# Kernel optimization log

Hardware: AMD Instinct MI355X
Metric: run time of the kernel (lower is better)

Reference implementation:

```python
import jax, jax.numpy as jnp
import numpy as np

N, E, F, C, ED, G, D = 50000, 1000000, 30, 64, 11, 1024, 256


def setup_inputs() -> dict:
    key = jax.random.key(0)
    ks = jax.random.split(key, 20)
    rn = lambda k, shape, s=0.1: jax.random.normal(k, shape, jnp.float32) * s
    return {
        "x": rn(ks[0], (N, F), 1.0),
        "edge_attr": jax.random.uniform(ks[1], (E, ED), jnp.float32),
        "W0": rn(ks[2], (F, C)), "asrc0": rn(ks[3], (C,)), "adst0": rn(ks[4], (C,)),
        "We0": rn(ks[5], (ED, C)), "ae0": rn(ks[6], (C,)), "Wres0": rn(ks[7], (F, C)),
        "b0": jnp.zeros((C,), jnp.float32),
        "W": rn(ks[8], (3, C, C)), "asrc": rn(ks[9], (3, C)), "adst": rn(ks[10], (3, C)),
        "We": rn(ks[11], (3, ED, C)), "ae": rn(ks[12], (3, C)), "Wres": rn(ks[13], (3, C, C)),
        "b": jnp.zeros((3, C), jnp.float32),
        "Wout": rn(ks[14], (2 * C, D)), "bout": jnp.zeros((D,), jnp.float32),
        "edge_index": jax.random.randint(ks[15], (2, E), 0, N),
        "batch_index": jnp.sort(jax.random.randint(ks[16], (N,), 0, G)),
    }


def _gat(x, src, dst, edge_attr, W, asrc, adst, We, ae, Wres, b):
    """PyG GATConv (heads=1) with edge_dim and residual=True."""
    n = x.shape[0]
    h = x @ W                                   # [N, C]
    e = edge_attr @ We                          # [E, C]
    alpha = (jnp.sum(h * asrc, -1)[src]
             + jnp.sum(h * adst, -1)[dst]
             + jnp.sum(e * ae, -1))             # [E]
    alpha = jax.nn.leaky_relu(alpha, 0.2)
    m = jax.ops.segment_max(alpha, dst, num_segments=n)
    a = jnp.exp(alpha - m[dst])
    s = jax.ops.segment_sum(a, dst, num_segments=n)
    a = a / (s[dst] + 1e-16)                    # per-dst softmax
    out = jax.ops.segment_sum(a[:, None] * h[src], dst, num_segments=n)
    return out + x @ Wres + b


def reference(x, edge_attr, W0, asrc0, adst0, We0, ae0, Wres0, b0,
              W, asrc, adst, We, ae, Wres, b, Wout, bout,
              edge_index, batch_index):
    src, dst = edge_index[0], edge_index[1]
    h = jax.nn.leaky_relu(
        _gat(x, src, dst, edge_attr, W0, asrc0, adst0, We0, ae0, Wres0, b0), 0.01)
    for i in range(3):  # conv1..conv3 (fixed small layer loop)
        h = _gat(h, src, dst, edge_attr, W[i], asrc[i], adst[i],
                 We[i], ae[i], Wres[i], b[i])
        if i < 2:
            h = jax.nn.leaky_relu(h, 0.01)
    gmax = jax.ops.segment_max(h, batch_index, num_segments=G)
    gmax = jnp.where(jnp.isfinite(gmax), gmax, 0.0)  # empty graphs -> 0
    cnt = jax.ops.segment_sum(jnp.ones((h.shape[0],), h.dtype), batch_index,
                              num_segments=G)
    gmean = jax.ops.segment_sum(h, batch_index, num_segments=G) / jnp.maximum(cnt, 1.0)[:, None]
    pooled = jax.nn.leaky_relu(jnp.concatenate([gmax, gmean], axis=1), 0.01)
    return pooled @ Wout + bout
```

## Files before the change

### kernel.cpp

```cpp
#include <hip/hip_runtime.h>
#include <hip/hip_fp16.h>

#define NN 50000
#define NE 1000000
#define FIN0 30
#define C 64
#define ED 11
#define NG 1024
#define DOUT 256
#define NBIN 196
#define PA_EDGES 1024

typedef unsigned long long ull;

__global__ __launch_bounds__(256) void hist196_kernel(const int* __restrict__ dst,
    int* __restrict__ bcnt){
  __shared__ int h[256];
  int t=threadIdx.x;
  h[t]=0;
  __syncthreads();
  for(int i=blockIdx.x*256+t;i<NE;i+=gridDim.x*256)
    atomicAdd(&h[dst[i]>>8],1);
  __syncthreads();
  if(h[t]) atomicAdd(&bcnt[t],h[t]);
}

__global__ __launch_bounds__(256) void scan196_kernel(const int* __restrict__ bcnt,
    int* __restrict__ bbase, int* __restrict__ gcur){
  __shared__ int p[256];
  int t=threadIdx.x;
  int v=bcnt[t];
  p[t]=v; __syncthreads();
  #pragma unroll
  for(int off=1;off<256;off<<=1){
    int u=(t>=off)?p[t-off]:0;
    __syncthreads(); p[t]+=u; __syncthreads();
  }
  int ex=p[t]-v;
  if(t<=NBIN) bbase[t]=ex;
  if(t<NBIN)  gcur[t]=ex;
}

__global__ __launch_bounds__(256) void grow_kernel(const int* __restrict__ batch,
    int* __restrict__ growptr){
  int i=blockIdx.x*256+threadIdx.x;
  if(i>=NN) return;
  int bi=batch[i];
  int bp=(i==0)?-1:batch[i-1];
  for(int g=bp+1;g<=bi;++g) growptr[g]=i;
  if(i==NN-1){ for(int g=bi+1;g<=NG;++g) growptr[g]=NN; }
}

__global__ __launch_bounds__(256) void part_kernel(const int* __restrict__ dst,
    const int* __restrict__ src, const float* __restrict__ edge_attr,
    const float* __restrict__ We0, const float* __restrict__ ae0,
    const float* __restrict__ We,  const float* __restrict__ ae,
    int* __restrict__ gcur, uint4* __restrict__ prec){
  __shared__ uint4 lrec[PA_EDGES];
  __shared__ float sw[4][ED];
  __shared__ int hist[256], sc[256], lofs[256], bb[256];
  __shared__ int wsum[4];
  int t=threadIdx.x;
  hist[t]=0;
  if(t<4*ED){
    int l=t/ED, j=t%ED;
    const float* wp=(l==0)? (We0+(size_t)j*C) : (We+((size_t)(l-1)*ED+j)*C);
    const float* ap=(l==0)? ae0 : (ae+(size_t)(l-1)*C);
    float s=0.f;
    for(int c=0;c<C;++c) s+=wp[c]*ap[c];
    sw[l][j]=s;
  }
  __syncthreads();
  size_t e0=(size_t)blockIdx.x*PA_EDGES;
  int cnt=(int)min((size_t)PA_EDGES,(size_t)NE-e0);
  int dreg[4], sreg[4];
  #pragma unroll
  for(int r=0;r<4;++r){
    int i=r*256+t;
    if(i<cnt){
      dreg[r]=dst[e0+i]; sreg[r]=src[e0+i];
      atomicAdd(&hist[dreg[r]>>8],1);
    } else dreg[r]=-1;
  }
  __syncthreads();
  int v=hist[t];
  int inc=v;
  #pragma unroll
  for(int off=1;off<64;off<<=1){
    int u=__shfl_up(inc,off,64);
    if((t&63)>=off) inc+=u;
  }
  if((t&63)==63) wsum[t>>6]=inc;
  __syncthreads();
  int woff=0;
  int myw=t>>6;
  #pragma unroll
  for(int k=0;k<3;++k) if(k<myw) woff+=wsum[k];
  int ex=woff+inc-v;
  sc[t]=ex;
  lofs[t]=ex;
  bb[t]=(v>0)?atomicAdd(&gcur[t],v):0;
  __syncthreads();
  #pragma unroll
  for(int r=0;r<4;++r){
    int i=r*256+t;
    if(i<cnt){
      const float* ea=edge_attr+(e0+i)*(size_t)ED;
      float d0=0,d1=0,d2=0,d3=0;
      #pragma unroll
      for(int j=0;j<ED;++j){
        float ev=ea[j];
        d0=fmaf(ev,sw[0][j],d0);
        d1=fmaf(ev,sw[1][j],d1);
        d2=fmaf(ev,sw[2][j],d2);
        d3=fmaf(ev,sw[3][j],d3);
      }
      uint4 rec;
      rec.x=(unsigned)dreg[r]; rec.y=(unsigned)sreg[r];
      rec.z=(unsigned)__half_as_ushort(__float2half(d0))
           |((unsigned)__half_as_ushort(__float2half(d1))<<16);
      rec.w=(unsigned)__half_as_ushort(__float2half(d2))
           |((unsigned)__half_as_ushort(__float2half(d3))<<16);
      int slot=atomicAdd(&lofs[dreg[r]>>8],1);
      lrec[slot]=rec;
    }
  }
  __syncthreads();
  for(int i=t;i<cnt;i+=256){
    uint4 rec=lrec[i];
    int b=(int)(rec.x>>8);
    int g=bb[b]+i-sc[b];
    prec[g]=rec;
  }
}

__global__ __launch_bounds__(256) void build_kernel(const uint4* __restrict__ prec,
    const int* __restrict__ bbase,
    int* __restrict__ rowptr, int* __restrict__ src_csr, ushort* __restrict__ edch){
  __shared__ int cnt[256], p[256], cur[256];
  int t=threadIdx.x, b=blockIdx.x;
  int n0=b<<8;
  cnt[t]=0;
  __syncthreads();
  int beg=bbase[b], endd=bbase[b+1];
  for(int j=beg+t;j<endd;j+=256)
    atomicAdd(&cnt[(int)prec[j].x-n0],1);
  __syncthreads();
  int v=cnt[t];
  p[t]=v; __syncthreads();
  #pragma unroll
  for(int off=1;off<256;off<<=1){
    int u=(t>=off)?p[t-off]:0;
    __syncthreads(); p[t]+=u; __syncthreads();
  }
  int ex=p[t]-v;
  cur[t]=beg+ex;
  if(n0+t<NN) rowptr[n0+t]=beg+ex;
  if(b==0&&t==0) rowptr[NN]=NE;
  __syncthreads();
  for(int j=beg+t;j<endd;j+=256){
    uint4 r=prec[j];
    int d=(int)r.x, s=(int)r.y;
    int pos=atomicAdd(&cur[d-n0],1);
    src_csr[pos]=s;
    edch[pos]                =(ushort)(r.z&0xffffu);
    edch[(size_t)NE+pos]     =(ushort)(r.z>>16);
    edch[2*(size_t)NE+pos]   =(ushort)(r.w&0xffffu);
    edch[3*(size_t)NE+pos]   =(ushort)(r.w>>16);
  }
}

template<int FIN, int SXS>
__global__ __launch_bounds__(256) void feat_kernel(const float* __restrict__ in,
    const float* __restrict__ W, const float* __restrict__ Wres,
    const float* __restrict__ bvec, const float* __restrict__ av_src,
    const float* __restrict__ av_dst,
    __half* __restrict__ hW16, float* __restrict__ outb,
    float* __restrict__ as_, float* __restrict__ ad_){
  __shared__ float sW[FIN*C], sR[FIN*C];
  __shared__ float sx[64*SXS];
  __shared__ float sb[C], ss[C], sd[C];
  int tid=threadIdx.x;
  if(tid<C){ sb[tid]=bvec[tid]; ss[tid]=av_src[tid]; sd[tid]=av_dst[tid]; }
  for(int i=tid;i<FIN*C;i+=256){ sW[i]=W[i]; sR[i]=Wres[i]; }
  int nbase=blockIdx.x*64;
  int nvalid=min(64,NN-nbase);
  if constexpr (FIN==64){
    const float4* in4=(const float4*)(in+(size_t)nbase*64);
    for(int i=tid;i<1024;i+=256){
      int n=i>>4, k=(i&15)*4;
      float4 v=(n<nvalid)?in4[i]:make_float4(0.f,0.f,0.f,0.f);
      *(float4*)&sx[n*SXS+k]=v;
    }
  } else {
    for(int i=tid;i<64*FIN;i+=256){
      int n=i/FIN, k=i-n*FIN;
      sx[n*SXS+k]=(n<nvalid)?in[(size_t)(nbase+n)*FIN+k]:0.f;
    }
  }
  __syncthreads();
  int w=tid>>6, lane=tid&63;
  int ng=lane>>4, cl=lane&15;
  int n0=w*16+ng*4;
  int c0=cl*4;
  float hw[4][4]={}, hr[4][4]={};
  const float* sxp=&sx[n0*SXS];
  #pragma unroll 2
  for(int k=0;k<FIN;k+=2){
    float4 wv0=*(const float4*)&sW[k*C+c0];
    float4 rv0=*(const float4*)&sR[k*C+c0];
    float4 wv1=*(const float4*)&sW[(k+1)*C+c0];
    float4 rv1=*(const float4*)&sR[(k+1)*C+c0];
    float2 x0=*(const float2*)&sxp[k];
    float2 x1=*(const float2*)&sxp[SXS+k];
    float2 x2=*(const float2*)&sxp[2*SXS+k];
    float2 x3=*(const float2*)&sxp[3*SXS+k];
    float xa[4]={x0.x,x1.x,x2.x,x3.x};
    float xb[4]={x0.y,x1.y,x2.y,x3.y};
    #pragma unroll
    for(int r=0;r<4;++r){
      hw[r][0]=fmaf(xa[r],wv0.x,hw[r][0]);
      hw[r][1]=fmaf(xa[r],wv0.y,hw[r][1]);
      hw[r][2]=fmaf(xa[r],wv0.z,hw[r][2]);
      hw[r][3]=fmaf(xa[r],wv0.w,hw[r][3]);
      hr[r][0]=fmaf(xa[r],rv0.x,hr[r][0]);
      hr[r][1]=fmaf(xa[r],rv0.y,hr[r][1]);
      hr[r][2]=fmaf(xa[r],rv0.z,hr[r][2]);
      hr[r][3]=fmaf(xa[r],rv0.w,hr[r][3]);
      hw[r][0]=fmaf(xb[r],wv1.x,hw[r][0]);
      hw[r][1]=fmaf(xb[r],wv1.y,hw[r][1]);
      hw[r][2]=fmaf(xb[r],wv1.z,hw[r][2]);
      hw[r][3]=fmaf(xb[r],wv1.w,hw[r][3]);
      hr[r][0]=fmaf(xb[r],rv1.x,hr[r][0]);
      hr[r][1]=fmaf(xb[r],rv1.y,hr[r][1]);
      hr[r][2]=fmaf(xb[r],rv1.z,hr[r][2]);
      hr[r][3]=fmaf(xb[r],rv1.w,hr[r][3]);
    }
  }
  float s0=ss[c0], s1=ss[c0+1], s2=ss[c0+2], s3=ss[c0+3];
  float d0=sd[c0], d1=sd[c0+1], d2=sd[c0+2], d3=sd[c0+3];
  float b0v=sb[c0], b1v=sb[c0+1], b2v=sb[c0+2], b3v=sb[c0+3];
  #pragma unroll
  for(int r=0;r<4;++r){
    int n=n0+r;
    float ps=hw[r][0]*s0+hw[r][1]*s1+hw[r][2]*s2+hw[r][3]*s3;
    float pd=hw[r][0]*d0+hw[r][1]*d1+hw[r][2]*d2+hw[r][3]*d3;
    #pragma unroll
    for(int off=1;off<16;off<<=1){ ps+=__shfl_xor(ps,off,64); pd+=__shfl_xor(pd,off,64); }
    if(n<nvalid){
      size_t gn=(size_t)(nbase+n);
      ushort4 hv;
      hv.x=__half_as_ushort(__float2half(hw[r][0]));
      hv.y=__half_as_ushort(__float2half(hw[r][1]));
      hv.z=__half_as_ushort(__float2half(hw[r][2]));
      hv.w=__half_as_ushort(__float2half(hw[r][3]));
      *(ushort4*)&hW16[gn*C+c0]=hv;
      float4 ov;
      ov.x=hr[r][0]+b0v; ov.y=hr[r][1]+b1v; ov.z=hr[r][2]+b2v; ov.w=hr[r][3]+b3v;
      *(float4*)&outb[gn*C+c0]=ov;
      if(cl==0){ as_[gn]=ps; ad_[gn]=pd; }
    }
  }
}

__device__ __forceinline__ void acc8(float* a, float at, uint4 u){
  __half2 h0=*(__half2*)&u.x, h1=*(__half2*)&u.y, h2=*(__half2*)&u.z, h3=*(__half2*)&u.w;
  float2 f0=__half22float2(h0), f1=__half22float2(h1);
  float2 f2=__half22float2(h2), f3=__half22float2(h3);
  a[0]=fmaf(at,f0.x,a[0]); a[1]=fmaf(at,f0.y,a[1]);
  a[2]=fmaf(at,f1.x,a[2]); a[3]=fmaf(at,f1.y,a[3]);
  a[4]=fmaf(at,f2.x,a[4]); a[5]=fmaf(at,f2.y,a[5]);
  a[6]=fmaf(at,f3.x,a[6]); a[7]=fmaf(at,f3.y,a[7]);
}

__global__ __launch_bounds__(256) void agg_kernel(const int* __restrict__ rowptr,
    const int* __restrict__ src_csr, const ushort* __restrict__ edc_l,
    const float* __restrict__ as_, const float* __restrict__ ad_,
    const __half* __restrict__ hW16, float* __restrict__ outb, int relu){
  __shared__ float2 sws[4][64];
  int w=threadIdx.x>>6, lane=threadIdx.x&63;
  int half=lane>>5, hl=lane&31;
  int n0=blockIdx.x*8+w*2;
  int nidx=n0+half;
  int beg=rowptr[nidx], end=rowptr[nidx+1];
  int deg=end-beg;
  const uint4* hw4=(const uint4*)hW16;

  if(__all(deg<=32)){
    float ad_n=ad_[nidx];
    int j=beg+hl;
    float al=-INFINITY; int sl=0;
    if(hl<deg){
      sl=src_csr[j];
      float a=as_[sl]+ad_n+__half2float(__ushort_as_half(edc_l[j]));
      al=(a>0.f)?a:0.2f*a;
    }
    float mn=al;
    #pragma unroll
    for(int off=16;off;off>>=1) mn=fmaxf(mn,__shfl_xor(mn,off,64));
    float wl=(hl<deg)?__expf(al-mn):0.f;
    float s=wl;
    #pragma unroll
    for(int off=16;off;off>>=1) s+=__shfl_xor(s,off,64);
    float2 pr; pr.x=wl; pr.y=__int_as_float(sl);
    sws[w][lane]=pr;
    int g=hl>>3, gl=hl&7;
    float acc[8]={0.f,0.f,0.f,0.f,0.f,0.f,0.f,0.f};
    int base=half*32;
    int t=g;
    for(; t+4<deg; t+=8){
      float2 r0=sws[w][base+t], r1=sws[w][base+t+4];
      uint4 u0=hw4[(size_t)__float_as_int(r0.y)*8+gl];
      uint4 u1=hw4[(size_t)__float_as_int(r1.y)*8+gl];
      acc8(acc,r0.x,u0);
      acc8(acc,r1.x,u1);
    }
    if(t<deg){
      float2 r=sws[w][base+t];
      uint4 u=hw4[(size_t)__float_as_int(r.y)*8+gl];
      acc8(acc,r.x,u);
    }
    #pragma unroll
    for(int off=8;off<=16;off<<=1){
      #pragma unroll
      for(int i=0;i<8;++i) acc[i]+=__shfl_xor(acc[i],off,64);
    }
    if(hl<8){
      float denom=s+1e-16f;
      size_t o0=(size_t)nidx*C+hl*8;
      float4 oa=*(float4*)&outb[o0];
      float4 ob=*(float4*)&outb[o0+4];
      float4 va,vb;
      va.x=acc[0]/denom+oa.x; va.y=acc[1]/denom+oa.y;
      va.z=acc[2]/denom+oa.z; va.w=acc[3]/denom+oa.w;
      vb.x=acc[4]/denom+ob.x; vb.y=acc[5]/denom+ob.y;
      vb.z=acc[6]/denom+ob.z; vb.w=acc[7]/denom+ob.w;
      if(relu){
        va.x=(va.x>0.f)?va.x:0.01f*va.x; va.y=(va.y>0.f)?va.y:0.01f*va.y;
        va.z=(va.z>0.f)?va.z:0.01f*va.z; va.w=(va.w>0.f)?va.w:0.01f*va.w;
        vb.x=(vb.x>0.f)?vb.x:0.01f*vb.x; vb.y=(vb.y>0.f)?vb.y:0.01f*vb.y;
        vb.z=(vb.z>0.f)?vb.z:0.01f*vb.z; vb.w=(vb.w>0.f)?vb.w:0.01f*vb.w;
      }
      *(float4*)&outb[o0]=va;
      *(float4*)&outb[o0+4]=vb;
    }
    return;
  }

  for(int h=0;h<2;++h){
    int m=n0+h;
    int bh=__shfl(beg,h*32,64);
    int dh=__shfl(deg,h*32,64);
    float ad_n=ad_[m];
    int g2=lane>>3, gl2=lane&7;
    float s=0.f;
    float acc[8]={0.f,0.f,0.f,0.f,0.f,0.f,0.f,0.f};
    if(dh<=64){
      int j=bh+lane;
      float al=-INFINITY; int sl=0;
      if(lane<dh){
        sl=src_csr[j];
        float a=as_[sl]+ad_n+__half2float(__ushort_as_half(edc_l[j]));
        al=(a>0.f)?a:0.2f*a;
      }
      float mn=al;
      #pragma unroll
      for(int off=32;off;off>>=1) mn=fmaxf(mn,__shfl_xor(mn,off,64));
      float wl=(lane<dh)?__expf(al-mn):0.f;
      s=wl;
      #pragma unroll
      for(int off=32;off;off>>=1) s+=__shfl_xor(s,off,64);
      float2 pr; pr.x=wl; pr.y=__int_as_float(sl);
      sws[w][lane]=pr;
      int t=g2;
      for(; t+8<dh; t+=16){
        float2 r0=sws[w][t], r1=sws[w][t+8];
        uint4 u0=hw4[(size_t)__float_as_int(r0.y)*8+gl2];
        uint4 u1=hw4[(size_t)__float_as_int(r1.y)*8+gl2];
        acc8(acc,r0.x,u0);
        acc8(acc,r1.x,u1);
      }
      if(t<dh){
        float2 r=sws[w][t];
        uint4 u=hw4[(size_t)__float_as_int(r.y)*8+gl2];
        acc8(acc,r.x,u);
      }
    } else {
      float m_=-INFINITY;
      for(int base=bh;base<bh+dh;base+=64){
        int j=base+lane;
        float al=-INFINITY; int sl=0;
        if(j<bh+dh){
          sl=src_csr[j];
          float a=as_[sl]+ad_n+__half2float(__ushort_as_half(edc_l[j]));
          al=(a>0.f)?a:0.2f*a;
        }
        float cm=al;
        #pragma unroll
        for(int off=32;off;off>>=1) cm=fmaxf(cm,__shfl_xor(cm,off,64));
        float mn=fmaxf(m_,cm);
        float scale=(m_==-INFINITY)?0.f:__expf(m_-mn);
        s*=scale;
        #pragma unroll
        for(int i=0;i<8;++i) acc[i]*=scale;
        float wl=(j<bh+dh)?__expf(al-mn):0.f;
        float cs=wl;
        #pragma unroll
        for(int off=32;off;off>>=1) cs+=__shfl_xor(cs,off,64);
        s+=cs; m_=mn;
        float2 pr; pr.x=wl; pr.y=__int_as_float(sl);
        sws[w][lane]=pr;
        int cnt=min(64,bh+dh-base);
        int t=g2;
        for(; t+8<cnt; t+=16){
          float2 r0=sws[w][t], r1=sws[w][t+8];
          uint4 u0=hw4[(size_t)__float_as_int(r0.y)*8+gl2];
          uint4 u1=hw4[(size_t)__float_as_int(r1.y)*8+gl2];
          acc8(acc,r0.x,u0);
          acc8(acc,r1.x,u1);
        }
        if(t<cnt){
          float2 r=sws[w][t];
          uint4 u=hw4[(size_t)__float_as_int(r.y)*8+gl2];
          acc8(acc,r.x,u);
        }
      }
    }
    #pragma unroll
    for(int off=8;off<64;off<<=1){
      #pragma unroll
      for(int i=0;i<8;++i) acc[i]+=__shfl_xor(acc[i],off,64);
    }
    if(g2==0){
      float denom=s+1e-16f;
      size_t o0=(size_t)m*C+gl2*8;
      float4 oa=*(float4*)&outb[o0];
      float4 ob=*(float4*)&outb[o0+4];
      float4 va,vb;
      va.x=acc[0]/denom+oa.x; va.y=acc[1]/denom+oa.y;
      va.z=acc[2]/denom+oa.z; va.w=acc[3]/denom+oa.w;
      vb.x=acc[4]/denom+ob.x; vb.y=acc[5]/denom+ob.y;
      vb.z=acc[6]/denom+ob.z; vb.w=acc[7]/denom+ob.w;
      if(relu){
        va.x=(va.x>0.f)?va.x:0.01f*va.x; va.y=(va.y>0.f)?va.y:0.01f*va.y;
        va.z=(va.z>0.f)?va.z:0.01f*va.z; va.w=(va.w>0.f)?va.w:0.01f*va.w;
        vb.x=(vb.x>0.f)?vb.x:0.01f*vb.x; vb.y=(vb.y>0.f)?vb.y:0.01f*vb.y;
        vb.z=(vb.z>0.f)?vb.z:0.01f*vb.z; vb.w=(vb.w>0.f)?vb.w:0.01f*vb.w;
      }
      *(float4*)&outb[o0]=va;
      *(float4*)&outb[o0+4]=vb;
    }
  }
}

__global__ __launch_bounds__(256) void pool_kernel(const float* __restrict__ h,
    const int* __restrict__ growptr, float* __restrict__ pooled){
  int w=threadIdx.x>>6, lane=threadIdx.x&63;
  int g=blockIdx.x*4+w;
  if(g>=NG) return;
  int beg=growptr[g], end=growptr[g+1];
  float mx=-INFINITY, sm=0.f;
  for(int n=beg;n<end;++n){ float v=h[(size_t)n*C+lane]; mx=fmaxf(mx,v); sm+=v; }
  int cnt=end-beg;
  float gm=(cnt==0)?0.f:mx;
  float mean=sm/fmaxf((float)cnt,1.f);
  gm=(gm>0.f)?gm:0.01f*gm;
  mean=(mean>0.f)?mean:0.01f*mean;
  pooled[(size_t)g*128+lane]=gm;
  pooled[(size_t)g*128+64+lane]=mean;
}

__global__ __launch_bounds__(256) void out_kernel(const float* __restrict__ pooled,
    const float* __restrict__ Wout, const float* __restrict__ bout,
    float* __restrict__ out){
  __shared__ float sp[128];
  int g=blockIdx.x, d=threadIdx.x;
  if(d<128) sp[d]=pooled[(size_t)g*128+d];
  __syncthreads();
  float o=bout[d];
  for(int k=0;k<128;++k) o=fmaf(sp[k],Wout[k*DOUT+d],o);
  out[(size_t)g*DOUT+d]=o;
}

extern "C" void kernel_launch(void* const* d_in, const int* in_sizes, int n_in,
                              void* d_out, int out_size, void* d_ws, size_t ws_size,
                              hipStream_t stream){
  const float* x        =(const float*)d_in[0];
  const float* edge_attr=(const float*)d_in[1];
  const float* W0       =(const float*)d_in[2];
  const float* asrc0    =(const float*)d_in[3];
  const float* adst0    =(const float*)d_in[4];
  const float* We0      =(const float*)d_in[5];
  const float* ae0      =(const float*)d_in[6];
  const float* Wres0    =(const float*)d_in[7];
  const float* b0       =(const float*)d_in[8];
  const float* W        =(const float*)d_in[9];
  const float* asrc     =(const float*)d_in[10];
  const float* adst     =(const float*)d_in[11];
  const float* We       =(const float*)d_in[12];
  const float* ae       =(const float*)d_in[13];
  const float* Wres     =(const float*)d_in[14];
  const float* b        =(const float*)d_in[15];
  const float* Wout     =(const float*)d_in[16];
  const float* bout     =(const float*)d_in[17];
  const int* edge_index =(const int*)d_in[18];
  const int* batch_index=(const int*)d_in[19];
  const int* src=edge_index;
  const int* dst=edge_index+NE;

  char* p=(char*)d_ws;
  auto take=[&](size_t bytes)->void*{ void* r=(void*)p; p+=(bytes+255)&~(size_t)255; return r; };
  int* rowptr  =(int*)take((size_t)(NN+1)*4);
  int* growptr =(int*)take((size_t)(NG+1)*4);
  int* bcnt    =(int*)take((size_t)256*4);
  int* bbase   =(int*)take((size_t)256*4);
  int* gcur    =(int*)take((size_t)256*4);
  int* src_csr =(int*)take((size_t)NE*4);
  float* as_   =(float*)take((size_t)NN*4);
  float* ad_   =(float*)take((size_t)NN*4);
  ushort* edch =(ushort*)take((size_t)NE*4*2);
  __half* hW16 =(__half*)take((size_t)NN*C*2);
  float* bufA  =(float*)take((size_t)NN*C*4);
  uint4* prec  =(uint4*)take((size_t)NE*16);
  float* bufB  =(float*)prec;
  float* pooled=(float*)take((size_t)NG*128*4);
  (void)ws_size; (void)in_sizes; (void)n_in; (void)out_size;

  hipMemsetAsync(bcnt,0,(size_t)256*4,stream);
  hist196_kernel<<<1024,256,0,stream>>>(dst,bcnt);
  scan196_kernel<<<1,256,0,stream>>>(bcnt,bbase,gcur);
  grow_kernel<<<(NN+255)/256,256,0,stream>>>(batch_index,growptr);

  part_kernel<<<(NE+PA_EDGES-1)/PA_EDGES,256,0,stream>>>(dst,src,edge_attr,
      We0,ae0,We,ae,gcur,prec);
  build_kernel<<<NBIN,256,0,stream>>>(prec,bbase,rowptr,src_csr,edch);

  const int nblkF=(NN+63)/64;
  const int nblkA=NN/8;
  feat_kernel<FIN0,36><<<nblkF,256,0,stream>>>(x,W0,Wres0,b0,asrc0,adst0,hW16,bufA,as_,ad_);
  agg_kernel<<<nblkA,256,0,stream>>>(rowptr,src_csr,edch,as_,ad_,hW16,bufA,1);
  float* bin=bufA; float* bo=bufB;
  for(int i=0;i<3;++i){
    feat_kernel<C,68><<<nblkF,256,0,stream>>>(bin,W+(size_t)i*C*C,Wres+(size_t)i*C*C,
        b+(size_t)i*C,asrc+(size_t)i*C,adst+(size_t)i*C,hW16,bo,as_,ad_);
    agg_kernel<<<nblkA,256,0,stream>>>(rowptr,src_csr,edch+(size_t)(i+1)*NE,as_,ad_,hW16,bo,(i<2)?1:0);
    float* t=bin; bin=bo; bo=t;
  }
  pool_kernel<<<(NG+3)/4,256,0,stream>>>(bin,growptr,pooled);
  out_kernel<<<NG,256,0,stream>>>(pooled,Wout,bout,(float*)d_out);
}
```

Before: 307.7 us.

## Split aggregation into softmax-weight kernel and channel-split gather kernel

Replaces the fused per-node softmax+gather aggregation with two kernels. One computes normalized edge weights into a global buffer, and the other gathers source features with the channel dimension split across two block halves, so each lane reads 32 of the 64 channels. The aim is more parallelism and simpler, more uniform gather loops. The cost is an extra kernel launch per layer, an extra write and read of a 4-byte weight per edge, and rowptr/src_csr being read twice. The partition kernel's edges per block are also halved.

```diff
diff --git a/kernel.cpp b/kernel.cpp
--- a/kernel.cpp
+++ b/kernel.cpp
@@ -9,7 +9,8 @@
 #define NG 1024
 #define DOUT 256
 #define NBIN 196
-#define PA_EDGES 1024
+#define PA_EDGES 512
+#define GHB (NN/8)
 
 typedef unsigned long long ull;
 
@@ -73,9 +74,9 @@
   __syncthreads();
   size_t e0=(size_t)blockIdx.x*PA_EDGES;
   int cnt=(int)min((size_t)PA_EDGES,(size_t)NE-e0);
-  int dreg[4], sreg[4];
-  #pragma unroll
-  for(int r=0;r<4;++r){
+  int dreg[2], sreg[2];
+  #pragma unroll
+  for(int r=0;r<2;++r){
     int i=r*256+t;
     if(i<cnt){
       dreg[r]=dst[e0+i]; sreg[r]=src[e0+i];
@@ -102,7 +103,7 @@
   bb[t]=(v>0)?atomicAdd(&gcur[t],v):0;
   __syncthreads();
   #pragma unroll
-  for(int r=0;r<4;++r){
+  for(int r=0;r<2;++r){
     int i=r*256+t;
     if(i<cnt){
       const float* ea=edge_attr+(e0+i)*(size_t)ED;
@@ -263,6 +264,79 @@
   }
 }
 
+__global__ __launch_bounds__(256) void wcalc_kernel(const int* __restrict__ rowptr,
+    const int* __restrict__ src_csr, const ushort* __restrict__ edc_l,
+    const float* __restrict__ as_, const float* __restrict__ ad_,
+    float* __restrict__ wgt){
+  int w=threadIdx.x>>6, lane=threadIdx.x&63;
+  int half=lane>>5, hl=lane&31;
+  int n0=blockIdx.x*8+w*2;
+  int nidx=n0+half;
+  int beg=rowptr[nidx], end=rowptr[nidx+1];
+  int deg=end-beg;
+
+  if(__all(deg<=32)){
+    int j=beg+hl;
+    float al=-INFINITY;
+    if(hl<deg){
+      int sl=src_csr[j];
+      float a=as_[sl]+ad_[nidx]+__half2float(__ushort_as_half(edc_l[j]));
+      al=(a>0.f)?a:0.2f*a;
+    }
+    float mn=al;
+    #pragma unroll
+    for(int off=16;off;off>>=1) mn=fmaxf(mn,__shfl_xor(mn,off,64));
+    float wl=(hl<deg)?__expf(al-mn):0.f;
+    float s=wl;
+    #pragma unroll
+    for(int off=16;off;off>>=1) s+=__shfl_xor(s,off,64);
+    if(hl<deg) wgt[j]=wl/(s+1e-16f);
+    return;
+  }
+
+  for(int h=0;h<2;++h){
+    int m=n0+h;
+    int bh=__shfl(beg,h*32,64);
+    int dh=__shfl(deg,h*32,64);
+    int eh=bh+dh;
+    float ad_n=ad_[m];
+    float mx=-INFINITY;
+    for(int base=bh;base<eh;base+=64){
+      int j=base+lane;
+      float al=-INFINITY;
+      if(j<eh){
+        int sl=src_csr[j];
+        float a=as_[sl]+ad_n+__half2float(__ushort_as_half(edc_l[j]));
+        al=(a>0.f)?a:0.2f*a;
+      }
+      #pragma unroll
+      for(int off=32;off;off>>=1) al=fmaxf(al,__shfl_xor(al,off,64));
+      mx=fmaxf(mx,al);
+    }
+    float s=0.f;
+    for(int base=bh;base<eh;base+=64){
+      int j=base+lane;
+      float wl=0.f;
+      if(j<eh){
+        int sl=src_csr[j];
+        float a=as_[sl]+ad_n+__half2float(__ushort_as_half(edc_l[j]));
+        float al=(a>0.f)?a:0.2f*a;
+        wl=__expf(al-mx);
+        wgt[j]=wl;
+      }
+      float cs=wl;
+      #pragma unroll
+      for(int off=32;off;off>>=1) cs+=__shfl_xor(cs,off,64);
+      s+=cs;
+    }
+    float inv=1.f/(s+1e-16f);
+    for(int base=bh;base<eh;base+=64){
+      int j=base+lane;
+      if(j<eh) wgt[j]*=inv;
+    }
+  }
+}
+
 __device__ __forceinline__ void acc8(float* a, float at, uint4 u){
   __half2 h0=*(__half2*)&u.x, h1=*(__half2*)&u.y, h2=*(__half2*)&u.z, h3=*(__half2*)&u.w;
   float2 f0=__half22float2(h0), f1=__half22float2(h1);
@@ -273,183 +347,57 @@
   a[6]=fmaf(at,f3.x,a[6]); a[7]=fmaf(at,f3.y,a[7]);
 }
 
-__global__ __launch_bounds__(256) void agg_kernel(const int* __restrict__ rowptr,
-    const int* __restrict__ src_csr, const ushort* __restrict__ edc_l,
-    const float* __restrict__ as_, const float* __restrict__ ad_,
+__global__ __launch_bounds__(256) void gath_kernel(const int* __restrict__ rowptr,
+    const int* __restrict__ src_csr, const float* __restrict__ wgt,
     const __half* __restrict__ hW16, float* __restrict__ outb, int relu){
-  __shared__ float2 sws[4][64];
   int w=threadIdx.x>>6, lane=threadIdx.x&63;
   int half=lane>>5, hl=lane&31;
-  int n0=blockIdx.x*8+w*2;
-  int nidx=n0+half;
-  int beg=rowptr[nidx], end=rowptr[nidx+1];
-  int deg=end-beg;
+  int cb=blockIdx.x;
+  int chalf=0;
+  if(cb>=GHB){ chalf=1; cb-=GHB; }
+  int nidx=cb*8+w*2+half;
+  int beg=rowptr[nidx];
+  int deg=rowptr[nidx+1]-beg;
+  int g=hl>>2, gl=hl&3;
   const uint4* hw4=(const uint4*)hW16;
-
-  if(__all(deg<=32)){
-    float ad_n=ad_[nidx];
-    int j=beg+hl;
-    float al=-INFINITY; int sl=0;
-    if(hl<deg){
-      sl=src_csr[j];
-      float a=as_[sl]+ad_n+__half2float(__ushort_as_half(edc_l[j]));
-      al=(a>0.f)?a:0.2f*a;
-    }
-    float mn=al;
+  size_t rowoff=(size_t)(chalf*4+gl);
+  float acc[8]={0.f,0.f,0.f,0.f,0.f,0.f,0.f,0.f};
+  int t=g;
+  for(; t+8<deg; t+=16){
+    int j0=beg+t, j1=beg+t+8;
+    float w0=wgt[j0], w1=wgt[j1];
+    int s0=src_csr[j0], s1=src_csr[j1];
+    uint4 u0=hw4[(size_t)s0*8+rowoff];
+    uint4 u1=hw4[(size_t)s1*8+rowoff];
+    acc8(acc,w0,u0);
+    acc8(acc,w1,u1);
+  }
+  if(t<deg){
+    int j=beg+t;
+    float wv=wgt[j]; int sv=src_csr[j];
+    uint4 u=hw4[(size_t)sv*8+rowoff];
+    acc8(acc,wv,u);
+  }
+  #pragma unroll
+  for(int off=4;off<=16;off<<=1){
     #pragma unroll
-    for(int off=16;off;off>>=1) mn=fmaxf(mn,__shfl_xor(mn,off,64));
-    float wl=(hl<deg)?__expf(al-mn):0.f;
-    float s=wl;
-    #pragma unroll
-    for(int off=16;off;off>>=1) s+=__shfl_xor(s,off,64);
-    float2 pr; pr.x=wl; pr.y=__int_as_float(sl);
-    sws[w][lane]=pr;
-    int g=hl>>3, gl=hl&7;
-    float acc[8]={0.f,0.f,0.f,0.f,0.f,0.f,0.f,0.f};
-    int base=half*32;
-    int t=g;
-    for(; t+4<deg; t+=8){
-      float2 r0=sws[w][base+t], r1=sws[w][base+t+4];
-      uint4 u0=hw4[(size_t)__float_as_int(r0.y)*8+gl];
-      uint4 u1=hw4[(size_t)__float_as_int(r1.y)*8+gl];
-      acc8(acc,r0.x,u0);
-      acc8(acc,r1.x,u1);
-    }
-    if(t<deg){
-      float2 r=sws[w][base+t];
-      uint4 u=hw4[(size_t)__float_as_int(r.y)*8+gl];
-      acc8(acc,r.x,u);
-    }
-    #pragma unroll
-    for(int off=8;off<=16;off<<=1){
-      #pragma unroll
-      for(int i=0;i<8;++i) acc[i]+=__shfl_xor(acc[i],off,64);
-    }
-    if(hl<8){
-      float denom=s+1e-16f;
-      size_t o0=(size_t)nidx*C+hl*8;
-      float4 oa=*(float4*)&outb[o0];
-      float4 ob=*(float4*)&outb[o0+4];
-      float4 va,vb;
-      va.x=acc[0]/denom+oa.x; va.y=acc[1]/denom+oa.y;
-      va.z=acc[2]/denom+oa.z; va.w=acc[3]/denom+oa.w;
-      vb.x=acc[4]/denom+ob.x; vb.y=acc[5]/denom+ob.y;
-      vb.z=acc[6]/denom+ob.z; vb.w=acc[7]/denom+ob.w;
-      if(relu){
-        va.x=(va.x>0.f)?va.x:0.01f*va.x; va.y=(va.y>0.f)?va.y:0.01f*va.y;
-        va.z=(va.z>0.f)?va.z:0.01f*va.z; va.w=(va.w>0.f)?va.w:0.01f*va.w;
-        vb.x=(vb.x>0.f)?vb.x:0.01f*vb.x; vb.y=(vb.y>0.f)?vb.y:0.01f*vb.y;
-        vb.z=(vb.z>0.f)?vb.z:0.01f*vb.z; vb.w=(vb.w>0.f)?vb.w:0.01f*vb.w;
-      }
-      *(float4*)&outb[o0]=va;
-      *(float4*)&outb[o0+4]=vb;
-    }
-    return;
-  }
-
-  for(int h=0;h<2;++h){
-    int m=n0+h;
-    int bh=__shfl(beg,h*32,64);
-    int dh=__shfl(deg,h*32,64);
-    float ad_n=ad_[m];
-    int g2=lane>>3, gl2=lane&7;
-    float s=0.f;
-    float acc[8]={0.f,0.f,0.f,0.f,0.f,0.f,0.f,0.f};
-    if(dh<=64){
-      int j=bh+lane;
-      float al=-INFINITY; int sl=0;
-      if(lane<dh){
-        sl=src_csr[j];
-        float a=as_[sl]+ad_n+__half2float(__ushort_as_half(edc_l[j]));
-        al=(a>0.f)?a:0.2f*a;
-      }
-      float mn=al;
-      #pragma unroll
-      for(int off=32;off;off>>=1) mn=fmaxf(mn,__shfl_xor(mn,off,64));
-      float wl=(lane<dh)?__expf(al-mn):0.f;
-      s=wl;
-      #pragma unroll
-      for(int off=32;off;off>>=1) s+=__shfl_xor(s,off,64);
-      float2 pr; pr.x=wl; pr.y=__int_as_float(sl);
-      sws[w][lane]=pr;
-      int t=g2;
-      for(; t+8<dh; t+=16){
-        float2 r0=sws[w][t], r1=sws[w][t+8];
-        uint4 u0=hw4[(size_t)__float_as_int(r0.y)*8+gl2];
-        uint4 u1=hw4[(size_t)__float_as_int(r1.y)*8+gl2];
-        acc8(acc,r0.x,u0);
-        acc8(acc,r1.x,u1);
-      }
-      if(t<dh){
-        float2 r=sws[w][t];
-        uint4 u=hw4[(size_t)__float_as_int(r.y)*8+gl2];
-        acc8(acc,r.x,u);
-      }
-    } else {
-      float m_=-INFINITY;
-      for(int base=bh;base<bh+dh;base+=64){
-        int j=base+lane;
-        float al=-INFINITY; int sl=0;
-        if(j<bh+dh){
-          sl=src_csr[j];
-          float a=as_[sl]+ad_n+__half2float(__ushort_as_half(edc_l[j]));
-          al=(a>0.f)?a:0.2f*a;
-        }
-        float cm=al;
-        #pragma unroll
-        for(int off=32;off;off>>=1) cm=fmaxf(cm,__shfl_xor(cm,off,64));
-        float mn=fmaxf(m_,cm);
-        float scale=(m_==-INFINITY)?0.f:__expf(m_-mn);
-        s*=scale;
-        #pragma unroll
-        for(int i=0;i<8;++i) acc[i]*=scale;
-        float wl=(j<bh+dh)?__expf(al-mn):0.f;
-        float cs=wl;
-        #pragma unroll
-        for(int off=32;off;off>>=1) cs+=__shfl_xor(cs,off,64);
-        s+=cs; m_=mn;
-        float2 pr; pr.x=wl; pr.y=__int_as_float(sl);
-        sws[w][lane]=pr;
-        int cnt=min(64,bh+dh-base);
-        int t=g2;
-        for(; t+8<cnt; t+=16){
-          float2 r0=sws[w][t], r1=sws[w][t+8];
-          uint4 u0=hw4[(size_t)__float_as_int(r0.y)*8+gl2];
-          uint4 u1=hw4[(size_t)__float_as_int(r1.y)*8+gl2];
-          acc8(acc,r0.x,u0);
-          acc8(acc,r1.x,u1);
-        }
-        if(t<cnt){
-          float2 r=sws[w][t];
-          uint4 u=hw4[(size_t)__float_as_int(r.y)*8+gl2];
-          acc8(acc,r.x,u);
-        }
-      }
-    }
-    #pragma unroll
-    for(int off=8;off<64;off<<=1){
-      #pragma unroll
-      for(int i=0;i<8;++i) acc[i]+=__shfl_xor(acc[i],off,64);
-    }
-    if(g2==0){
-      float denom=s+1e-16f;
-      size_t o0=(size_t)m*C+gl2*8;
-      float4 oa=*(float4*)&outb[o0];
-      float4 ob=*(float4*)&outb[o0+4];
-      float4 va,vb;
-      va.x=acc[0]/denom+oa.x; va.y=acc[1]/denom+oa.y;
-      va.z=acc[2]/denom+oa.z; va.w=acc[3]/denom+oa.w;
-      vb.x=acc[4]/denom+ob.x; vb.y=acc[5]/denom+ob.y;
-      vb.z=acc[6]/denom+ob.z; vb.w=acc[7]/denom+ob.w;
-      if(relu){
-        va.x=(va.x>0.f)?va.x:0.01f*va.x; va.y=(va.y>0.f)?va.y:0.01f*va.y;
-        va.z=(va.z>0.f)?va.z:0.01f*va.z; va.w=(va.w>0.f)?va.w:0.01f*va.w;
-        vb.x=(vb.x>0.f)?vb.x:0.01f*vb.x; vb.y=(vb.y>0.f)?vb.y:0.01f*vb.y;
-        vb.z=(vb.z>0.f)?vb.z:0.01f*vb.z; vb.w=(vb.w>0.f)?vb.w:0.01f*vb.w;
-      }
-      *(float4*)&outb[o0]=va;
-      *(float4*)&outb[o0+4]=vb;
-    }
+    for(int i=0;i<8;++i) acc[i]+=__shfl_xor(acc[i],off,64);
+  }
+  if(hl<4){
+    size_t o0=(size_t)nidx*C+chalf*32+hl*8;
+    float4 oa=*(float4*)&outb[o0];
+    float4 ob=*(float4*)&outb[o0+4];
+    float4 va,vb;
+    va.x=acc[0]+oa.x; va.y=acc[1]+oa.y; va.z=acc[2]+oa.z; va.w=acc[3]+oa.w;
+    vb.x=acc[4]+ob.x; vb.y=acc[5]+ob.y; vb.z=acc[6]+ob.z; vb.w=acc[7]+ob.w;
+    if(relu){
+      va.x=(va.x>0.f)?va.x:0.01f*va.x; va.y=(va.y>0.f)?va.y:0.01f*va.y;
+      va.z=(va.z>0.f)?va.z:0.01f*va.z; va.w=(va.w>0.f)?va.w:0.01f*va.w;
+      vb.x=(vb.x>0.f)?vb.x:0.01f*vb.x; vb.y=(vb.y>0.f)?vb.y:0.01f*vb.y;
+      vb.z=(vb.z>0.f)?vb.z:0.01f*vb.z; vb.w=(vb.w>0.f)?vb.w:0.01f*vb.w;
+    }
+    *(float4*)&outb[o0]=va;
+    *(float4*)&outb[o0+4]=vb;
   }
 }
 
@@ -518,6 +466,7 @@
   int* src_csr =(int*)take((size_t)NE*4);
   float* as_   =(float*)take((size_t)NN*4);
   float* ad_   =(float*)take((size_t)NN*4);
+  float* wgt   =(float*)take((size_t)NE*4);
   ushort* edch =(ushort*)take((size_t)NE*4*2);
   __half* hW16 =(__half*)take((size_t)NN*C*2);
   float* bufA  =(float*)take((size_t)NN*C*4);
@@ -536,14 +485,15 @@
   build_kernel<<<NBIN,256,0,stream>>>(prec,bbase,rowptr,src_csr,edch);
 
   const int nblkF=(NN+63)/64;
-  const int nblkA=NN/8;
   feat_kernel<FIN0,36><<<nblkF,256,0,stream>>>(x,W0,Wres0,b0,asrc0,adst0,hW16,bufA,as_,ad_);
-  agg_kernel<<<nblkA,256,0,stream>>>(rowptr,src_csr,edch,as_,ad_,hW16,bufA,1);
+  wcalc_kernel<<<GHB,256,0,stream>>>(rowptr,src_csr,edch,as_,ad_,wgt);
+  gath_kernel<<<2*GHB,256,0,stream>>>(rowptr,src_csr,wgt,hW16,bufA,1);
   float* bin=bufA; float* bo=bufB;
   for(int i=0;i<3;++i){
     feat_kernel<C,68><<<nblkF,256,0,stream>>>(bin,W+(size_t)i*C*C,Wres+(size_t)i*C*C,
         b+(size_t)i*C,asrc+(size_t)i*C,adst+(size_t)i*C,hW16,bo,as_,ad_);
-    agg_kernel<<<nblkA,256,0,stream>>>(rowptr,src_csr,edch+(size_t)(i+1)*NE,as_,ad_,hW16,bo,(i<2)?1:0);
+    wcalc_kernel<<<GHB,256,0,stream>>>(rowptr,src_csr,edch+(size_t)(i+1)*NE,as_,ad_,wgt);
+    gath_kernel<<<2*GHB,256,0,stream>>>(rowptr,src_csr,wgt,hW16,bo,(i<2)?1:0);
     float* t=bin; bin=bo; bo=t;
   }
   pool_kernel<<<(NG+3)/4,256,0,stream>>>(bin,growptr,pooled);
```

New measurement: 383.1 us. +24.5%, slower.
